# Performance work log

Measured on AMD Instinct MI355X. Metric: run time of the kernel, lower is better.

Reference implementation:

```python
import jax, jax.numpy as jnp
import numpy as np

N_NODES = 100000
N_EDGES = 800000
N_GRAPHS = 64
N_ETYPES = 4
D = 150
HID = 512
PASSES = 5


def setup_inputs() -> dict:
    key = jax.random.key(0)
    ks = jax.random.split(key, 16)
    s = 0.1
    return {
        "nodes": jax.random.normal(ks[0], (N_NODES, D), jnp.float32),
        "problem_class": jax.random.normal(ks[1], (N_GRAPHS, 1), jnp.float32),
        "edge_src": jax.random.randint(ks[2], (N_EDGES,), 0, N_NODES, jnp.int32),
        "edge_dst": jax.random.randint(ks[3], (N_EDGES,), 0, N_NODES, jnp.int32),
        "edge_type": jax.random.randint(ks[4], (N_EDGES,), 0, N_ETYPES, jnp.int32),
        "graph_ids": jnp.sort(jax.random.randint(ks[5], (N_NODES,), 0, N_GRAPHS, jnp.int32)),
        "W_e": jax.random.normal(ks[6], (N_ETYPES, D, D), jnp.float32) * s,
        "b_e": jax.random.normal(ks[7], (N_ETYPES, D), jnp.float32) * s,
        "w_ih": jax.random.normal(ks[8], (3 * D, D), jnp.float32) * s,
        "w_hh": jax.random.normal(ks[9], (3 * D, D), jnp.float32) * s,
        "b_ih": jax.random.normal(ks[10], (3 * D,), jnp.float32) * s,
        "b_hh": jax.random.normal(ks[11], (3 * D,), jnp.float32) * s,
        "fc1_w": jax.random.normal(ks[12], (D + 1, HID), jnp.float32) * s,
        "fc1_b": jax.random.normal(ks[13], (HID,), jnp.float32) * s,
        "fc2_w": jax.random.normal(ks[14], (HID, 10), jnp.float32) * s,
        "fc2_b": jax.random.normal(ks[15], (10,), jnp.float32) * s,
    }


def _gru_cell(x, h, w_ih, w_hh, b_ih, b_hh):
    # torch.nn.GRUCell math, gate order (r, z, n)
    gi = x @ w_ih.T + b_ih
    gh = h @ w_hh.T + b_hh
    i_r, i_z, i_n = jnp.split(gi, 3, axis=1)
    h_r, h_z, h_n = jnp.split(gh, 3, axis=1)
    r = jax.nn.sigmoid(i_r + h_r)
    z = jax.nn.sigmoid(i_z + h_z)
    n = jnp.tanh(i_n + r * h_n)
    return (1.0 - z) * n + z * h


def reference(nodes, problem_class, edge_src, edge_dst, edge_type, graph_ids,
              W_e, b_e, w_ih, w_hh, b_ih, b_hh, fc1_w, fc1_b, fc2_w, fc2_b):
    n_nodes = nodes.shape[0]
    n_graphs = problem_class.shape[0]
    n_types = W_e.shape[0]

    # in-degree per edge type (for the per-edge Linear bias contribution)
    type_onehot = jax.nn.one_hot(edge_type, n_types, dtype=nodes.dtype)  # [E, T]
    deg = jax.ops.segment_sum(type_onehot, edge_dst, num_segments=n_nodes)  # [N, T]
    bias_inc = deg @ b_e  # [N, D] = sum_t deg_t * b_t

    h = nodes
    for _ in range(PASSES):
        h_src = h[edge_src]  # [E, D] gather
        inc = bias_inc
        for t in range(n_types):
            # aggregate first, apply the edge-type Linear after (linearity)
            agg = jax.ops.segment_sum(
                jnp.where((edge_type == t)[:, None], h_src, 0.0),
                edge_dst, num_segments=n_nodes)  # [N, D]
            inc = inc + agg @ W_e[t].T
        h = _gru_cell(inc, h, w_ih, w_hh, b_ih, b_hh)

    # graph readout: sum nodes, log, nan -> 0, relu
    g = jax.ops.segment_sum(h, graph_ids, num_segments=n_graphs)  # [B, D]
    l = jnp.log(g)
    l = jax.nn.relu(jnp.where(jnp.isnan(l), 0.0, l))
    x = jnp.concatenate([l, problem_class], axis=1)  # [B, D+1]
    x = jax.nn.leaky_relu(x @ fc1_w + fc1_b)
    return x @ fc2_w + fc2_b
```

## Files before the change

### kernel.cpp

```cpp
#include <hip/hip_runtime.h>
#include <hip/hip_bf16.h>
#include <cstdint>
#include <cstddef>

#define NN 100000
#define NE 800000
#define NG 64
#define NT 4
#define DD 150
#define HS 160
#define HIDN 512
#define NPASS 5
#define NBINS (NN*NT)
#define RPB 16

typedef short  s8v  __attribute__((ext_vector_type(8)));
typedef float  f32x4 __attribute__((ext_vector_type(4)));

static __device__ __forceinline__ float sigmoidf_(float x){ return 1.f/(1.f+expf(-x)); }
static __device__ __forceinline__ short f2bf(float x){
  __hip_bfloat16 b = __float2bfloat16(x);
  return *(short*)&b;
}
static __device__ __forceinline__ float bf2f(short s){
  union { unsigned u; float f; } v; v.u = ((unsigned)(unsigned short)s) << 16; return v.f;
}
static __device__ __forceinline__ void split_bf(float x, short& hi, short& lo){
  hi = f2bf(x);
  lo = f2bf(x - bf2f(hi));
}

static __device__ __forceinline__ void stage16(const unsigned short* __restrict__ g,
                                               short* l, int tid){
  const int wave = tid >> 6, lane = tid & 63;
  #pragma unroll
  for (int k2 = 0; k2 < 5; k2++){
    const int cb = k2*256 + wave*64;
    const unsigned short* gp = g + (size_t)(cb + lane)*8;
    short* lp = l + (size_t)cb*8;
    __builtin_amdgcn_global_load_lds(
        (const __attribute__((address_space(1))) void*)gp,
        (__attribute__((address_space(3))) void*)lp, 16, 0, 0);
  }
}


__global__ void count_kernel(const int* __restrict__ dst, const int* __restrict__ typ,
                             unsigned* __restrict__ deg){
  int e = blockIdx.x*256 + threadIdx.x;
  if (e < NE) atomicAdd(&deg[dst[e]*NT + typ[e]], 1u);
}

__device__ unsigned block_excl_base(unsigned threadSum){
  const int tid = threadIdx.x;
  const int lane = tid & 63, wid = tid >> 6;
  unsigned s = threadSum;
  #pragma unroll
  for (int d = 1; d < 64; d <<= 1){ unsigned t = __shfl_up(s, d); if (lane >= d) s += t; }
  __shared__ unsigned wsum[4];
  if (lane == 63) wsum[wid] = s;
  __syncthreads();
  unsigned base = 0;
  for (int w = 0; w < wid; w++) base += wsum[w];
  return base + s - threadSum;
}

__global__ void scan_reduce(const unsigned* __restrict__ deg, unsigned* __restrict__ bsum){
  const int base = blockIdx.x*1024 + threadIdx.x*4;
  unsigned s = 0;
  #pragma unroll
  for (int i = 0; i < 4; i++){ const int idx = base+i; if (idx < NBINS) s += deg[idx]; }
  #pragma unroll
  for (int d = 1; d < 64; d <<= 1) s += __shfl_down(s, d);
  __shared__ unsigned ws4[4];
  const int lane = threadIdx.x & 63, wid = threadIdx.x >> 6;
  if (lane == 0) ws4[wid] = s;
  __syncthreads();
  if (threadIdx.x == 0) bsum[blockIdx.x] = ws4[0]+ws4[1]+ws4[2]+ws4[3];
}

__global__ void scan_block(unsigned* bsum, int n){
  const int tid = threadIdx.x;
  unsigned v[4]; unsigned s = 0;
  #pragma unroll
  for (int i = 0; i < 4; i++){ const int idx = tid*4+i; v[i] = (idx < n) ? bsum[idx] : 0u; s += v[i]; }
  unsigned run = block_excl_base(s);
  #pragma unroll
  for (int i = 0; i < 4; i++){ const int idx = tid*4+i; if (idx < n) bsum[idx] = run; run += v[i]; }
}

__global__ void scan_final(const unsigned* __restrict__ deg, const unsigned* __restrict__ bsum,
                           unsigned* __restrict__ off){
  const int tid = threadIdx.x;
  const int base0 = blockIdx.x*1024 + tid*4;
  unsigned v[4]; unsigned s = 0;
  #pragma unroll
  for (int i = 0; i < 4; i++){ const int idx = base0+i; v[i] = (idx < NBINS) ? deg[idx] : 0u; s += v[i]; }
  unsigned run = block_excl_base(s) + bsum[blockIdx.x];
  #pragma unroll
  for (int i = 0; i < 4; i++){ const int idx = base0+i; if (idx < NBINS) off[idx] = run; run += v[i]; }
  if (blockIdx.x == 0 && tid == 0) off[NBINS] = NE;
}

__global__ void scatter_sort(const int* __restrict__ src, const int* __restrict__ dst,
                             const int* __restrict__ typ, unsigned* __restrict__ cur,
                             int* __restrict__ srcSorted){
  int e = blockIdx.x*256 + threadIdx.x;
  if (e < NE){
    const int bin = dst[e]*NT + typ[e];
    const unsigned p = atomicAdd(&cur[bin], 1u);
    srcSorted[p] = src[e];
  }
}

__global__ void init_h(const float* __restrict__ nodes, float* __restrict__ h0){
  const long long idx = (long long)blockIdx.x*256 + threadIdx.x;
  if (idx >= (long long)NN*HS) return;
  const int row = (int)(idx / HS), col = (int)(idx % HS);
  float v = 0.f;
  if (col < DD) v = nodes[(size_t)row*DD + col];
  h0[idx] = v;
}

__global__ void build_bfrag_msg(const float* __restrict__ W, unsigned short* __restrict__ out){
  const int idx = blockIdx.x*256 + threadIdx.x;
  if (idx >= NT*5*10*2*512) return;
  const int w = idx & 511;
  int r = idx >> 9;
  const int c = r % 2;  r /= 2;
  const int i = r % 10; r /= 10;
  const int s = r % 5;  const int t = r / 5;
  const int l = w >> 3, j = w & 7;
  const int n  = 16*i + (l & 15);
  const int kk = 32*s + (l >> 4)*8 + j;
  float v = 0.f;
  if (n < DD && kk < DD) v = W[(size_t)(t*DD + n)*DD + kk];
  short hi, lo; split_bf(v, hi, lo);
  out[(size_t)((t*5 + s)*20 + i*2 + c)*512 + w] = (unsigned short)(c ? lo : hi);
}

__global__ void build_bfrag_gru(const float* __restrict__ w_ih, const float* __restrict__ w_hh,
                                unsigned short* __restrict__ out){
  const int idx = blockIdx.x*256 + threadIdx.x;
  if (idx >= 10*3*2*2*5*512) return;
  const int w = idx & 511;
  int r = idx >> 9;
  const int s = r % 5;    r /= 5;
  const int c = r % 2;    r /= 2;
  const int u = r % 2;    r /= 2;
  const int part = r % 3; const int iT = r / 3;
  const int P = part*2 + u;
  const int g = P >> 1;
  const float* W = (P & 1) ? w_hh : w_ih;
  const int l = w >> 3, j = w & 7;
  const int n  = 16*iT + (l & 15);
  const int kk = 32*s + (l >> 4)*8 + j;
  float v = 0.f;
  if (n < DD && kk < DD) v = W[(size_t)(g*DD + n)*DD + kk];
  short hi, lo; split_bf(v, hi, lo);
  out[(size_t)((iT*3 + part)*20 + u*10 + c*5 + s)*512 + w] = (unsigned short)(c ? lo : hi);
}

#define MFMA3(acc, ahi, alo, bhi, blo) \
  acc = __builtin_amdgcn_mfma_f32_16x16x32_bf16(ahi, bhi, acc, 0,0,0); \
  acc = __builtin_amdgcn_mfma_f32_16x16x32_bf16(alo, bhi, acc, 0,0,0); \
  acc = __builtin_amdgcn_mfma_f32_16x16x32_bf16(ahi, blo, acc, 0,0,0);

__global__ __launch_bounds__(256, 2) void msg_kernel(
    const float* __restrict__ h, const int* __restrict__ srcS,
    const unsigned* __restrict__ off, const unsigned* __restrict__ deg,
    const float* __restrict__ b_e,
    const unsigned short* __restrict__ BfE2,
    float* __restrict__ inc)
{
  __shared__ short Bs[2][20*512];
  const int tid = threadIdx.x, wave = tid >> 6, l = tid & 63;
  const int m = l & 15, q = l >> 4, q8 = q*8;
  const int arow = blockIdx.x*64 + wave*16 + m;
  const bool av = (arow < NN);
  const int lb8 = l*8;

  f32x4 acc[10];
  #pragma unroll
  for (int i = 0; i < 10; i++) acc[i] = (f32x4)(0.0f);

  stage16(BfE2,          &Bs[0][0], tid);
  stage16(BfE2 + 10240,  &Bs[1][0], tid);
  __syncthreads();

  for (int t = 0; t < NT; t++){
    if (t > 0) stage16(BfE2 + (size_t)(t*5 + 1)*10240, &Bs[(t*5+1) & 1][0], tid);

    float a[5][8];
    #pragma unroll
    for (int s = 0; s < 5; s++)
      #pragma unroll
      for (int j = 0; j < 8; j++) a[s][j] = 0.f;

    int lo = 0, hi = 0;
    if (av){ const int bin = arow*NT + t; lo = (int)off[bin]; hi = (int)off[bin+1]; }
    int e = lo;
    int i0 = (e   < hi) ? srcS[e]   : 0;
    int i1 = (e+1 < hi) ? srcS[e+1] : -1;
    while (e < hi){
      const int n0 = (e+2 < hi) ? srcS[e+2] : 0;
      const int n1 = (e+3 < hi) ? srcS[e+3] : -1;
      const float* p0 = h + (size_t)i0*HS + q8;
      const float* p1 = h + (size_t)(i1 < 0 ? 0 : i1)*HS + q8;
      const float w1 = (i1 < 0) ? 0.f : 1.f;
      f32x4 v[10], u[10];
      #pragma unroll
      for (int s = 0; s < 5; s++){
        v[2*s]   = *(const f32x4*)(p0 + 32*s);
        v[2*s+1] = *(const f32x4*)(p0 + 32*s + 4);
      }
      #pragma unroll
      for (int s = 0; s < 5; s++){
        u[2*s]   = *(const f32x4*)(p1 + 32*s);
        u[2*s+1] = *(const f32x4*)(p1 + 32*s + 4);
      }
      #pragma unroll
      for (int s = 0; s < 5; s++){
        #pragma unroll
        for (int j = 0; j < 4; j++){
          a[s][j]   += v[2*s][j];
          a[s][j]   = fmaf(w1, u[2*s][j], a[s][j]);
          a[s][4+j] += v[2*s+1][j];
          a[s][4+j] = fmaf(w1, u[2*s+1][j], a[s][4+j]);
        }
      }
      e += 2; i0 = n0; i1 = n1;
    }

    s8v af_hi[5], af_lo[5];
    #pragma unroll
    for (int s = 0; s < 5; s++)
      #pragma unroll
      for (int j = 0; j < 8; j++){
        short h2, l2; split_bf(a[s][j], h2, l2);
        af_hi[s][j] = h2; af_lo[s][j] = l2;
      }

    #pragma unroll
    for (int st = 0; st < 5; st++){
      const int sidx = t*5 + st;
      if (st >= 1 && sidx + 1 < 20)
        stage16(BfE2 + (size_t)(sidx+1)*10240, &Bs[(sidx+1) & 1][0], tid);
      const short* bsr = &Bs[sidx & 1][0];
      #pragma unroll
      for (int i = 0; i < 10; i++){
        const s8v bh = *(const s8v*)(bsr + (i*2+0)*512 + lb8);
        const s8v bl = *(const s8v*)(bsr + (i*2+1)*512 + lb8);
        MFMA3(acc[i], af_hi[st], af_lo[st], bh, bl)
      }
      __syncthreads();
    }
  }

  const int crow0 = blockIdx.x*64 + wave*16 + q*4;
  #pragma unroll
  for (int r = 0; r < 4; r++){
    const int crow = crow0 + r;
    if (crow < NN){
      const uint4 dg = *(const uint4*)(&deg[crow*NT]);
      const float d0=(float)dg.x, d1=(float)dg.y, d2=(float)dg.z, d3=(float)dg.w;
      float* op = inc + (size_t)crow*HS;
      #pragma unroll
      for (int i = 0; i < 10; i++){
        const int c = 16*i + m;
        float val = 0.f;
        if (c < DD)
          val = acc[i][r] + fmaf(d0, b_e[c], fmaf(d1, b_e[DD+c],
                  fmaf(d2, b_e[2*DD+c], d3*b_e[3*DD+c])));
        op[c] = val;
      }
    }
  }
}

__global__ __launch_bounds__(256, 2) void gru_kernel(
    const float* __restrict__ h, float* __restrict__ incnext,
    const unsigned short* __restrict__ BfG,
    const float* __restrict__ b_ih, const float* __restrict__ b_hh)
{
  __shared__ short Bs[2][20*512];
  const int tid = threadIdx.x, wave = tid >> 6, l = tid & 63;
  const int m = l & 15, q = l >> 4, q8 = q*8;
  const int arow = blockIdx.x*64 + wave*16 + m;
  const bool av = (arow < NN);
  const int lb8 = l*8;
  const int crow0 = blockIdx.x*64 + wave*16 + q*4;

  stage16(BfG, &Bs[0][0], tid);

  s8v afi_h[5], afi_l[5], afh_h[5], afh_l[5];
  {
    const float* ip = incnext + (size_t)(av ? arow : 0)*HS;
    const float* hp = h       + (size_t)(av ? arow : 0)*HS;
    #pragma unroll
    for (int s = 0; s < 5; s++){
      const int b = 32*s + q8;
      const f32x4 x0 = *(const f32x4*)(ip + b), x1 = *(const f32x4*)(ip + b + 4);
      const f32x4 y0 = *(const f32x4*)(hp + b), y1 = *(const f32x4*)(hp + b + 4);
      #pragma unroll
      for (int j = 0; j < 4; j++){
        short h2, l2;
        split_bf(x0[j], h2, l2); afi_h[s][j]   = h2; afi_l[s][j]   = l2;
        split_bf(x1[j], h2, l2); afi_h[s][4+j] = h2; afi_l[s][4+j] = l2;
        split_bf(y0[j], h2, l2); afh_h[s][j]   = h2; afh_l[s][j]   = l2;
        split_bf(y1[j], h2, l2); afh_h[s][4+j] = h2; afh_l[s][4+j] = l2;
      }
    }
  }
  __syncthreads();

  f32x4 aR=(f32x4)(0.f), aZ=(f32x4)(0.f);
  float hv[4] = {0.f,0.f,0.f,0.f};

  for (int k = 0; k < 30; k++){
    if (k + 1 < 30) stage16(BfG + (size_t)(k+1)*10240, &Bs[(k+1) & 1][0], tid);

    const int iT = k/3, part = k - 3*iT;
    const int d = 16*iT + m;
    if (part == 0){
      #pragma unroll
      for (int r = 0; r < 4; r++){
        hv[r] = 0.f;
        if (crow0 + r < NN && d < DD) hv[r] = h[(size_t)(crow0+r)*HS + d];
      }
    }

    const short* bsr = &Bs[k & 1][0];
    f32x4 tI = (f32x4)(0.f), tH = (f32x4)(0.f);
    #pragma unroll
    for (int s = 0; s < 5; s++){
      const s8v b0h = *(const s8v*)(bsr + (     s)*512 + lb8);
      const s8v b0l = *(const s8v*)(bsr + ( 5 + s)*512 + lb8);
      const s8v b1h = *(const s8v*)(bsr + (10 + s)*512 + lb8);
      const s8v b1l = *(const s8v*)(bsr + (15 + s)*512 + lb8);
      MFMA3(tI, afi_h[s], afi_l[s], b0h, b0l)
      MFMA3(tH, afh_h[s], afh_l[s], b1h, b1l)
    }

    if (part == 0){
      aR = tI + tH;
    } else if (part == 1){
      aZ = tI + tH;
    } else if (d < DD){
      const float br   = b_ih[d]    + b_hh[d];
      const float bz   = b_ih[DD+d] + b_hh[DD+d];
      const float bin2 = b_ih[2*DD+d];
      const float bhn  = b_hh[2*DD+d];
      #pragma unroll
      for (int r = 0; r < 4; r++){
        const int crow = crow0 + r;
        if (crow < NN){
          const float rr = sigmoidf_(aR[r] + br);
          const float zz = sigmoidf_(aZ[r] + bz);
          const float nn = tanhf(tI[r] + bin2 + rr*(tH[r] + bhn));
          incnext[(size_t)crow*HS + d] = (1.f - zz)*nn + zz*hv[r];
        }
      }
    }
    __syncthreads();
  }
}

__global__ void readout1(const float* __restrict__ h, const int* __restrict__ gids,
                         float* __restrict__ part){
  const int g = blockIdx.x >> 4, s = blockIdx.x & (RPB-1);
  const int tid = threadIdx.x;
  __shared__ int sb[2];
  if (tid < 2){
    const int target = g + tid;
    int lo = 0, hi = NN;
    while (lo < hi){ const int mid = (lo+hi) >> 1; if (gids[mid] < target) lo = mid+1; else hi = mid; }
    sb[tid] = lo;
  }
  __syncthreads();
  const int lo = sb[0], hi = sb[1];
  const int len = hi - lo;
  const int per = (len + RPB - 1) / RPB;
  const int nlo = lo + s*per;
  const int nhi = (nlo + per < hi) ? (nlo + per) : hi;
  if (tid < DD){
    float acc = 0.f;
    for (int n = nlo; n < nhi; n++) acc += h[(size_t)n*HS + tid];
    part[(size_t)blockIdx.x*DD + tid] = acc;
  }
}

__global__ void readout2(const float* __restrict__ part, const float* __restrict__ pclass,
                         float* __restrict__ xbuf){
  const int g = blockIdx.x, tid = threadIdx.x;
  if (tid < DD){
    float acc = 0.f;
    #pragma unroll
    for (int s = 0; s < RPB; s++) acc += part[(size_t)(g*RPB + s)*DD + tid];
    float l = logf(acc);
    if (isnan(l)) l = 0.f;
    l = fmaxf(l, 0.f);
    xbuf[g*(DD+1)+tid] = l;
  }
  if (tid == DD) xbuf[g*(DD+1)+DD] = pclass[g];
}

__global__ void fc1_kernel(const float* __restrict__ xbuf, const float* __restrict__ w,
                           const float* __restrict__ b, float* __restrict__ hid){
  const int g = blockIdx.x, tid = threadIdx.x;
  __shared__ float xs[DD+1];
  if (tid < DD+1) xs[tid] = xbuf[g*(DD+1)+tid];
  __syncthreads();
  float acc = b[tid];
  for (int k = 0; k < DD+1; k++) acc = fmaf(xs[k], w[k*HIDN + tid], acc);
  hid[g*HIDN + tid] = (acc > 0.f) ? acc : 0.01f*acc;
}

__global__ void fc2_kernel(const float* __restrict__ hid, const float* __restrict__ w,
                           const float* __restrict__ b, float* __restrict__ out){
  const int g = blockIdx.x, tid = threadIdx.x;
  __shared__ float hs[HIDN];
  for (int i = tid; i < HIDN; i += 64) hs[i] = hid[g*HIDN + i];
  __syncthreads();
  if (tid < 10){
    float acc = b[tid];
    for (int k = 0; k < HIDN; k++) acc = fmaf(hs[k], w[k*10 + tid], acc);
    out[g*10 + tid] = acc;
  }
}

extern "C" void kernel_launch(void* const* d_in, const int* in_sizes, int n_in,
                              void* d_out, int out_size, void* d_ws, size_t ws_size,
                              hipStream_t stream)
{
  (void)in_sizes; (void)n_in; (void)out_size; (void)ws_size;
  const float* nodes  = (const float*)d_in[0];
  const float* pclass = (const float*)d_in[1];
  const int*   esrc   = (const int*)d_in[2];
  const int*   edst   = (const int*)d_in[3];
  const int*   etyp   = (const int*)d_in[4];
  const int*   gids   = (const int*)d_in[5];
  const float* W_e    = (const float*)d_in[6];
  const float* b_e    = (const float*)d_in[7];
  const float* w_ih   = (const float*)d_in[8];
  const float* w_hh   = (const float*)d_in[9];
  const float* b_ih   = (const float*)d_in[10];
  const float* b_hh   = (const float*)d_in[11];
  const float* fc1w   = (const float*)d_in[12];
  const float* fc1b   = (const float*)d_in[13];
  const float* fc2w   = (const float*)d_in[14];
  const float* fc2b   = (const float*)d_in[15];
  float* out = (float*)d_out;

  char* p = (char*)d_ws;
  auto alloc = [&](size_t bytes)->char* {
    char* r = p; p += ((bytes + 255) & ~(size_t)255); return r;
  };
  float*    h0   = (float*)alloc((size_t)NN*HS*4);
  float*    h1   = (float*)alloc((size_t)NN*HS*4);
  unsigned* deg  = (unsigned*)alloc((size_t)NBINS*4);
  unsigned* off  = (unsigned*)alloc((size_t)(NBINS+1)*4);
  unsigned* cur  = (unsigned*)alloc((size_t)NBINS*4);
  unsigned* bsum = (unsigned*)alloc(4096);
  int*      srcS = (int*)alloc((size_t)NE*4);
  unsigned short* BfE2 = (unsigned short*)alloc((size_t)20*20*512*2);
  unsigned short* BfG  = (unsigned short*)alloc((size_t)30*20*512*2);
  float*    part = (float*)alloc((size_t)NG*RPB*DD*4);
  float*    xbuf = (float*)alloc((size_t)NG*(DD+1)*4);
  float*    hidb = (float*)alloc((size_t)NG*HIDN*4);

  hipMemsetAsync(deg, 0, (size_t)NBINS*4, stream);
  count_kernel<<<(NE+255)/256, 256, 0, stream>>>(edst, etyp, deg);
  const int SCB = (NBINS + 1023)/1024;
  scan_reduce<<<SCB, 256, 0, stream>>>(deg, bsum);
  scan_block<<<1, 256, 0, stream>>>(bsum, SCB);
  scan_final<<<SCB, 256, 0, stream>>>(deg, bsum, off);
  hipMemcpyAsync(cur, off, (size_t)NBINS*4, hipMemcpyDeviceToDevice, stream);
  scatter_sort<<<(NE+255)/256, 256, 0, stream>>>(esrc, edst, etyp, cur, srcS);
  build_bfrag_msg<<<(NT*5*10*2*512+255)/256, 256, 0, stream>>>(W_e, BfE2);
  build_bfrag_gru<<<(10*3*2*2*5*512+255)/256, 256, 0, stream>>>(w_ih, w_hh, BfG);
  init_h<<<(int)(((long long)NN*HS + 255)/256), 256, 0, stream>>>(nodes, h0);

  float* hb[2] = {h0, h1};
  const int grows = (NN + 63)/64;
  for (int pass = 0; pass < NPASS; pass++){
    const float* hc = hb[pass & 1];
    float*       hn = hb[(pass + 1) & 1];
    msg_kernel<<<grows, 256, 0, stream>>>(hc, srcS, off, deg, b_e, BfE2, hn);
    gru_kernel<<<grows, 256, 0, stream>>>(hc, hn, BfG, b_ih, b_hh);
  }

  readout1<<<NG*RPB, 256, 0, stream>>>(hb[NPASS & 1], gids, part);
  readout2<<<NG, 256, 0, stream>>>(part, pclass, xbuf);
  fc1_kernel<<<NG, HIDN, 0, stream>>>(xbuf, fc1w, fc1b, hidb);
  fc2_kernel<<<NG, 64, 0, stream>>>(hidb, fc2w, fc2b, out);
}
```

Before: 1.818 ms.

## Split bf16 weight fragments into hi/lo arrays, stage only hi in LDS

Weight fragments for the message and GRU matmuls are now stored as separate hi and lo bf16 arrays. Only the hi part is staged through LDS, which halves shared memory per block. The lo-correction fragments are read directly from global memory (expected to hit in cache) in a separate MFMA loop. The msg kernel also loads all five CSR offsets for its row once, instead of two offsets per edge type. This trades LDS footprint and staging traffic for extra global loads on the lo path.

```diff
diff --git a/kernel.cpp b/kernel.cpp
--- a/kernel.cpp
+++ b/kernel.cpp
@@ -30,17 +30,19 @@
   lo = f2bf(x - bf2f(hi));
 }
 
-static __device__ __forceinline__ void stage16(const unsigned short* __restrict__ g,
+static __device__ __forceinline__ void stage10(const unsigned short* __restrict__ g,
                                                short* l, int tid){
   const int wave = tid >> 6, lane = tid & 63;
   #pragma unroll
-  for (int k2 = 0; k2 < 5; k2++){
+  for (int k2 = 0; k2 < 3; k2++){
     const int cb = k2*256 + wave*64;
-    const unsigned short* gp = g + (size_t)(cb + lane)*8;
-    short* lp = l + (size_t)cb*8;
-    __builtin_amdgcn_global_load_lds(
-        (const __attribute__((address_space(1))) void*)gp,
-        (__attribute__((address_space(3))) void*)lp, 16, 0, 0);
+    if (cb < 640){
+      const unsigned short* gp = g + (size_t)(cb + lane)*8;
+      short* lp = l + (size_t)cb*8;
+      __builtin_amdgcn_global_load_lds(
+          (const __attribute__((address_space(1))) void*)gp,
+          (__attribute__((address_space(3))) void*)lp, 16, 0, 0);
+    }
   }
 }
 
@@ -122,12 +124,13 @@
   h0[idx] = v;
 }
 
-__global__ void build_bfrag_msg(const float* __restrict__ W, unsigned short* __restrict__ out){
+__global__ void build_bfrag_msg(const float* __restrict__ W,
+                                unsigned short* __restrict__ outh,
+                                unsigned short* __restrict__ outl){
   const int idx = blockIdx.x*256 + threadIdx.x;
-  if (idx >= NT*5*10*2*512) return;
+  if (idx >= NT*5*10*512) return;
   const int w = idx & 511;
   int r = idx >> 9;
-  const int c = r % 2;  r /= 2;
   const int i = r % 10; r /= 10;
   const int s = r % 5;  const int t = r / 5;
   const int l = w >> 3, j = w & 7;
@@ -136,18 +139,20 @@
   float v = 0.f;
   if (n < DD && kk < DD) v = W[(size_t)(t*DD + n)*DD + kk];
   short hi, lo; split_bf(v, hi, lo);
-  out[(size_t)((t*5 + s)*20 + i*2 + c)*512 + w] = (unsigned short)(c ? lo : hi);
+  const size_t o = (size_t)((t*5 + s)*10 + i)*512 + w;
+  outh[o] = (unsigned short)hi;
+  outl[o] = (unsigned short)lo;
 }
 
 __global__ void build_bfrag_gru(const float* __restrict__ w_ih, const float* __restrict__ w_hh,
-                                unsigned short* __restrict__ out){
+                                unsigned short* __restrict__ outh,
+                                unsigned short* __restrict__ outl){
   const int idx = blockIdx.x*256 + threadIdx.x;
-  if (idx >= 10*3*2*2*5*512) return;
+  if (idx >= 30*10*512) return;
   const int w = idx & 511;
   int r = idx >> 9;
-  const int s = r % 5;    r /= 5;
-  const int c = r % 2;    r /= 2;
-  const int u = r % 2;    r /= 2;
+  const int s = r % 5;  r /= 5;
+  const int u = r % 2;  r /= 2;
   const int part = r % 3; const int iT = r / 3;
   const int P = part*2 + u;
   const int g = P >> 1;
@@ -158,22 +163,19 @@
   float v = 0.f;
   if (n < DD && kk < DD) v = W[(size_t)(g*DD + n)*DD + kk];
   short hi, lo; split_bf(v, hi, lo);
-  out[(size_t)((iT*3 + part)*20 + u*10 + c*5 + s)*512 + w] = (unsigned short)(c ? lo : hi);
-}
-
-#define MFMA3(acc, ahi, alo, bhi, blo) \
-  acc = __builtin_amdgcn_mfma_f32_16x16x32_bf16(ahi, bhi, acc, 0,0,0); \
-  acc = __builtin_amdgcn_mfma_f32_16x16x32_bf16(alo, bhi, acc, 0,0,0); \
-  acc = __builtin_amdgcn_mfma_f32_16x16x32_bf16(ahi, blo, acc, 0,0,0);
+  const size_t o = (size_t)((iT*3 + part)*10 + u*5 + s)*512 + w;
+  outh[o] = (unsigned short)hi;
+  outl[o] = (unsigned short)lo;
+}
 
 __global__ __launch_bounds__(256, 2) void msg_kernel(
     const float* __restrict__ h, const int* __restrict__ srcS,
     const unsigned* __restrict__ off, const unsigned* __restrict__ deg,
     const float* __restrict__ b_e,
-    const unsigned short* __restrict__ BfE2,
+    const unsigned short* __restrict__ BfEh, const unsigned short* __restrict__ BfEl,
     float* __restrict__ inc)
 {
-  __shared__ short Bs[2][20*512];
+  __shared__ short Bs[2][10*512];
   const int tid = threadIdx.x, wave = tid >> 6, l = tid & 63;
   const int m = l & 15, q = l >> 4, q8 = q*8;
   const int arow = blockIdx.x*64 + wave*16 + m;
@@ -184,12 +186,19 @@
   #pragma unroll
   for (int i = 0; i < 10; i++) acc[i] = (f32x4)(0.0f);
 
-  stage16(BfE2,          &Bs[0][0], tid);
-  stage16(BfE2 + 10240,  &Bs[1][0], tid);
+  unsigned ob0=0, ob1=0, ob2=0, ob3=0, ob4=0;
+  if (av){
+    const uint4 ob = *(const uint4*)&off[arow*NT];
+    ob0=ob.x; ob1=ob.y; ob2=ob.z; ob3=ob.w;
+    ob4 = off[arow*NT + 4];
+  }
+
+  stage10(BfEh,         &Bs[0][0], tid);
+  stage10(BfEh + 5120,  &Bs[1][0], tid);
   __syncthreads();
 
   for (int t = 0; t < NT; t++){
-    if (t > 0) stage16(BfE2 + (size_t)(t*5 + 1)*10240, &Bs[(t*5+1) & 1][0], tid);
+    if (t > 0) stage10(BfEh + (size_t)(t*5 + 1)*5120, &Bs[(t*5+1) & 1][0], tid);
 
     float a[5][8];
     #pragma unroll
@@ -197,8 +206,8 @@
       #pragma unroll
       for (int j = 0; j < 8; j++) a[s][j] = 0.f;
 
-    int lo = 0, hi = 0;
-    if (av){ const int bin = arow*NT + t; lo = (int)off[bin]; hi = (int)off[bin+1]; }
+    const int lo = (int)((t==0)?ob0:(t==1)?ob1:(t==2)?ob2:ob3);
+    const int hi = (int)((t==0)?ob1:(t==1)?ob2:(t==2)?ob3:ob4);
     int e = lo;
     int i0 = (e   < hi) ? srcS[e]   : 0;
     int i1 = (e+1 < hi) ? srcS[e+1] : -1;
@@ -245,13 +254,19 @@
     for (int st = 0; st < 5; st++){
       const int sidx = t*5 + st;
       if (st >= 1 && sidx + 1 < 20)
-        stage16(BfE2 + (size_t)(sidx+1)*10240, &Bs[(sidx+1) & 1][0], tid);
+        stage10(BfEh + (size_t)(sidx+1)*5120, &Bs[(sidx+1) & 1][0], tid);
       const short* bsr = &Bs[sidx & 1][0];
+      const unsigned short* blg = BfEl + (size_t)sidx*5120 + lb8;
       #pragma unroll
       for (int i = 0; i < 10; i++){
-        const s8v bh = *(const s8v*)(bsr + (i*2+0)*512 + lb8);
-        const s8v bl = *(const s8v*)(bsr + (i*2+1)*512 + lb8);
-        MFMA3(acc[i], af_hi[st], af_lo[st], bh, bl)
+        const s8v bh = *(const s8v*)(bsr + i*512 + lb8);
+        acc[i] = __builtin_amdgcn_mfma_f32_16x16x32_bf16(af_hi[st], bh, acc[i], 0,0,0);
+        acc[i] = __builtin_amdgcn_mfma_f32_16x16x32_bf16(af_lo[st], bh, acc[i], 0,0,0);
+      }
+      #pragma unroll
+      for (int i = 0; i < 10; i++){
+        const s8v bl = *(const s8v*)(blg + (size_t)i*512);
+        acc[i] = __builtin_amdgcn_mfma_f32_16x16x32_bf16(af_hi[st], bl, acc[i], 0,0,0);
       }
       __syncthreads();
     }
@@ -280,10 +295,10 @@
 
 __global__ __launch_bounds__(256, 2) void gru_kernel(
     const float* __restrict__ h, float* __restrict__ incnext,
-    const unsigned short* __restrict__ BfG,
+    const unsigned short* __restrict__ BfGh, const unsigned short* __restrict__ BfGl,
     const float* __restrict__ b_ih, const float* __restrict__ b_hh)
 {
-  __shared__ short Bs[2][20*512];
+  __shared__ short Bs[2][10*512];
   const int tid = threadIdx.x, wave = tid >> 6, l = tid & 63;
   const int m = l & 15, q = l >> 4, q8 = q*8;
   const int arow = blockIdx.x*64 + wave*16 + m;
@@ -291,7 +306,7 @@
   const int lb8 = l*8;
   const int crow0 = blockIdx.x*64 + wave*16 + q*4;
 
-  stage16(BfG, &Bs[0][0], tid);
+  stage10(BfGh, &Bs[0][0], tid);
 
   s8v afi_h[5], afi_l[5], afh_h[5], afh_l[5];
   {
@@ -318,7 +333,7 @@
   float hv[4] = {0.f,0.f,0.f,0.f};
 
   for (int k = 0; k < 30; k++){
-    if (k + 1 < 30) stage16(BfG + (size_t)(k+1)*10240, &Bs[(k+1) & 1][0], tid);
+    if (k + 1 < 30) stage10(BfGh + (size_t)(k+1)*5120, &Bs[(k+1) & 1][0], tid);
 
     const int iT = k/3, part = k - 3*iT;
     const int d = 16*iT + m;
@@ -331,15 +346,23 @@
     }
 
     const short* bsr = &Bs[k & 1][0];
+    const unsigned short* blg = BfGl + (size_t)k*5120 + lb8;
     f32x4 tI = (f32x4)(0.f), tH = (f32x4)(0.f);
     #pragma unroll
     for (int s = 0; s < 5; s++){
-      const s8v b0h = *(const s8v*)(bsr + (     s)*512 + lb8);
-      const s8v b0l = *(const s8v*)(bsr + ( 5 + s)*512 + lb8);
-      const s8v b1h = *(const s8v*)(bsr + (10 + s)*512 + lb8);
-      const s8v b1l = *(const s8v*)(bsr + (15 + s)*512 + lb8);
-      MFMA3(tI, afi_h[s], afi_l[s], b0h, b0l)
-      MFMA3(tH, afh_h[s], afh_l[s], b1h, b1l)
+      const s8v b0h = *(const s8v*)(bsr + (    s)*512 + lb8);
+      const s8v b1h = *(const s8v*)(bsr + (5 + s)*512 + lb8);
+      tI = __builtin_amdgcn_mfma_f32_16x16x32_bf16(afi_h[s], b0h, tI, 0,0,0);
+      tI = __builtin_amdgcn_mfma_f32_16x16x32_bf16(afi_l[s], b0h, tI, 0,0,0);
+      tH = __builtin_amdgcn_mfma_f32_16x16x32_bf16(afh_h[s], b1h, tH, 0,0,0);
+      tH = __builtin_amdgcn_mfma_f32_16x16x32_bf16(afh_l[s], b1h, tH, 0,0,0);
+    }
+    #pragma unroll
+    for (int s = 0; s < 5; s++){
+      const s8v b0l = *(const s8v*)(blg + (size_t)(    s)*512);
+      const s8v b1l = *(const s8v*)(blg + (size_t)(5 + s)*512);
+      tI = __builtin_amdgcn_mfma_f32_16x16x32_bf16(afi_h[s], b0l, tI, 0,0,0);
+      tH = __builtin_amdgcn_mfma_f32_16x16x32_bf16(afh_h[s], b1l, tH, 0,0,0);
     }
 
     if (part == 0){
@@ -463,8 +486,10 @@
   unsigned* cur  = (unsigned*)alloc((size_t)NBINS*4);
   unsigned* bsum = (unsigned*)alloc(4096);
   int*      srcS = (int*)alloc((size_t)NE*4);
-  unsigned short* BfE2 = (unsigned short*)alloc((size_t)20*20*512*2);
-  unsigned short* BfG  = (unsigned short*)alloc((size_t)30*20*512*2);
+  unsigned short* BfEh = (unsigned short*)alloc((size_t)20*10*512*2);
+  unsigned short* BfEl = (unsigned short*)alloc((size_t)20*10*512*2);
+  unsigned short* BfGh = (unsigned short*)alloc((size_t)30*10*512*2);
+  unsigned short* BfGl = (unsigned short*)alloc((size_t)30*10*512*2);
   float*    part = (float*)alloc((size_t)NG*RPB*DD*4);
   float*    xbuf = (float*)alloc((size_t)NG*(DD+1)*4);
   float*    hidb = (float*)alloc((size_t)NG*HIDN*4);
@@ -477,8 +502,8 @@
   scan_final<<<SCB, 256, 0, stream>>>(deg, bsum, off);
   hipMemcpyAsync(cur, off, (size_t)NBINS*4, hipMemcpyDeviceToDevice, stream);
   scatter_sort<<<(NE+255)/256, 256, 0, stream>>>(esrc, edst, etyp, cur, srcS);
-  build_bfrag_msg<<<(NT*5*10*2*512+255)/256, 256, 0, stream>>>(W_e, BfE2);
-  build_bfrag_gru<<<(10*3*2*2*5*512+255)/256, 256, 0, stream>>>(w_ih, w_hh, BfG);
+  build_bfrag_msg<<<(NT*5*10*512+255)/256, 256, 0, stream>>>(W_e, BfEh, BfEl);
+  build_bfrag_gru<<<(30*10*512+255)/256, 256, 0, stream>>>(w_ih, w_hh, BfGh, BfGl);
   init_h<<<(int)(((long long)NN*HS + 255)/256), 256, 0, stream>>>(nodes, h0);
 
   float* hb[2] = {h0, h1};
@@ -486,8 +511,8 @@
   for (int pass = 0; pass < NPASS; pass++){
     const float* hc = hb[pass & 1];
     float*       hn = hb[(pass + 1) & 1];
-    msg_kernel<<<grows, 256, 0, stream>>>(hc, srcS, off, deg, b_e, BfE2, hn);
-    gru_kernel<<<grows, 256, 0, stream>>>(hc, hn, BfG, b_ih, b_hh);
+    msg_kernel<<<grows, 256, 0, stream>>>(hc, srcS, off, deg, b_e, BfEh, BfEl, hn);
+    gru_kernel<<<grows, 256, 0, stream>>>(hc, hn, BfGh, BfGl, b_ih, b_hh);
   }
 
   readout1<<<NG*RPB, 256, 0, stream>>>(hb[NPASS & 1], gids, part);
```

Result: slower. 2.514 ms (+38.2%).
